# Kernel optimization log

Measured on AMD Instinct MI355X. Metric: run time of the kernel, lower is better.

Reference implementation:

```python
import jax, jax.numpy as jnp
import numpy as np

B, S, D, H = 4, 2048, 512, 8
DEPTH = D // H


def setup_inputs() -> dict:
    key = jax.random.key(0)
    ks = jax.random.split(key, 12)
    scale = 0.02
    inp = {
        "q": jax.random.normal(ks[0], (B, S, D), dtype=jnp.float32),
        "k": jax.random.normal(ks[1], (B, S, D), dtype=jnp.float32),
        "v": jax.random.normal(ks[2], (B, S, D), dtype=jnp.float32),
        "mask": jax.random.randint(ks[3], (B, S, S), 0, 2, dtype=jnp.int32),
        "wq": jax.random.normal(ks[4], (D, D), dtype=jnp.float32) * scale,
        "bq": jnp.zeros((D,), dtype=jnp.float32),
        "wk": jax.random.normal(ks[5], (D, D), dtype=jnp.float32) * scale,
        "bk": jnp.zeros((D,), dtype=jnp.float32),
        "wv": jax.random.normal(ks[6], (D, D), dtype=jnp.float32) * scale,
        "bv": jnp.zeros((D,), dtype=jnp.float32),
        "wo": jax.random.normal(ks[7], (D, D), dtype=jnp.float32) * scale,
        "bo": jnp.zeros((D,), dtype=jnp.float32),
    }
    return inp


def _split_heads(x):
    # [B, S, D] -> [B, H, S, depth]
    b, s, _ = x.shape
    return x.reshape(b, s, H, DEPTH).transpose(0, 2, 1, 3)


def reference(q, k, v, mask, wq, bq, wk, bk, wv, bv, wo, bo):
    qh = _split_heads(q @ wq + bq)
    kh = _split_heads(k @ wk + bk)
    vh = _split_heads(v @ wv + bv)
    # scaled dot-product attention with additive mask, materializing [B,H,S,S]
    scores = jnp.einsum("bhqd,bhkd->bhqk", qh, kh) / jnp.sqrt(
        jnp.asarray(DEPTH, jnp.float32)
    )
    scores = scores + mask[:, None, :, :].astype(jnp.float32) * (-1e9)
    w = jax.nn.softmax(scores, axis=-1)
    o = jnp.einsum("bhqk,bhkd->bhqd", w, vh)
    o = o.transpose(0, 2, 1, 3).reshape(q.shape[0], -1, D)  # [B, S, D]
    return o @ wo + bo
```

## Files before the change

kernel.cpp:

```cpp
#include <hip/hip_runtime.h>
#include <hip/hip_bf16.h>
#include <stdint.h>

#define B_ 4
#define S_ 2048
#define D_ 512
#define H_ 8

typedef __attribute__((ext_vector_type(8))) short short8;
typedef __attribute__((ext_vector_type(4))) float f32x4;
typedef __attribute__((ext_vector_type(4))) unsigned short u16x4;

#define MFMA16(a,b,c) __builtin_amdgcn_mfma_f32_16x16x32_bf16((a),(b),(c),0,0,0)

__device__ __forceinline__ unsigned short f2bf(float f){
    return __builtin_bit_cast(unsigned short, __float2bfloat16(f));
}

__device__ __forceinline__ float maskf(float p, uint32_t keep){
    return __builtin_bit_cast(float, __builtin_bit_cast(uint32_t, p) & keep);
}

__device__ __forceinline__ float max3f(float a, float b, float c){
    float d;
    asm("v_max3_f32 %0, %1, %2, %3" : "=v"(d) : "v"(a), "v"(b), "v"(c));
    return d;
}

__device__ __forceinline__ void gload_lds16(const void* g, void* l){
    __builtin_amdgcn_global_load_lds((const __attribute__((address_space(1))) uint32_t*)g,
                                     (__attribute__((address_space(3))) uint32_t*)l, 16, 0, 0);
}

__global__ __launch_bounds__(256) void maskpack_kernel(const int* __restrict__ mask,
                                                       uint32_t* __restrict__ out)
{
    int idx = blockIdx.x*256 + threadIdx.x;
    const int4* p = (const int4*)(mask + (size_t)idx*32);
    uint32_t bits = 0;
    #pragma unroll
    for (int c=0;c<8;c++){
        int4 v = p[c];
        if (v.x) bits |= 1u << (c*4+0);
        if (v.y) bits |= 1u << (c*4+1);
        if (v.z) bits |= 1u << (c*4+2);
        if (v.w) bits |= 1u << (c*4+3);
    }
    out[idx] = bits;
}

__global__ __launch_bounds__(256) void wtrans_kernel(const float* __restrict__ wq,
                                                     const float* __restrict__ wk,
                                                     const float* __restrict__ wv,
                                                     const float* __restrict__ wo,
                                                     unsigned short* __restrict__ wt)
{
    int f = (blockIdx.x*256 + threadIdx.x) * 8;
    int mat = f >> 18;
    int rem = f & 262143;
    const float* Wm = (mat==0)?wq:(mat==1)?wk:(mat==2)?wv:wo;
    int nn = rem >> 9, kk0 = rem & 511;
    short8 o;
    #pragma unroll
    for (int j=0;j<8;j++)
        o[j] = (short)f2bf(Wm[(size_t)(kk0+j)*512 + nn]);
    *(short8*)(wt + (size_t)mat*262144 + (size_t)nn*512 + kk0) = o;
}

__global__ __launch_bounds__(256) void proj_kernel(
    const float* __restrict__ q, const float* __restrict__ k, const float* __restrict__ v,
    const float* __restrict__ bq, const float* __restrict__ bk, const float* __restrict__ bv,
    const unsigned short* __restrict__ wt, unsigned short* __restrict__ outb)
{
    __shared__ uint8_t smem[16384];
    const int t = threadIdx.x, l = t&63, w = t>>6, g = l>>4, ln = l&15;
    const int z = blockIdx.z;
    const float* X = (z==0)? q : (z==1)? k : v;
    const float* bias = (z==0)? bq : (z==1)? bk : bv;
    const unsigned short* WTz = wt + (size_t)z*(D_*D_);
    unsigned short* out = outb + (size_t)z*((size_t)B_*H_*S_*64);
    const float scale = (z==0)? 0.18033688011112042f : 1.0f;
    const int m0 = blockIdx.x*128, n0 = blockIdx.y*128;
    uint8_t* As = smem; uint8_t* Bs = smem + 8192;
    const int RB = (w>>1)*64, CB = (w&1)*64;

    const f32x4 zz = {0.f,0.f,0.f,0.f};
    f32x4 acc[4][4];
    #pragma unroll
    for (int i=0;i<4;i++)
        #pragma unroll
        for (int j=0;j<4;j++) acc[i][j] = zz;

    for (int k0=0; k0<D_; k0+=32){
        __syncthreads();
        #pragma unroll
        for (int i=0;i<2;i++){
            int qc = w + i*4;
            int row = qc*16 + (l>>2);
            int colb = ((l&3)*16) ^ ((row&3)<<4);
            gload_lds16((const uint8_t*)WTz + (((size_t)(n0+row)*D_ + k0)<<1) + colb,
                        Bs + qc*1024);
        }
        #pragma unroll
        for (int i=0;i<2;i++){
            int c = t + i*256;
            int row = c>>2, cc = c&3;
            const float4* src = (const float4*)(X + (size_t)(m0+row)*D_ + k0 + cc*8);
            float4 u0 = src[0], u1 = src[1];
            uint32_t c0,c1,c2,c3;
            asm("v_cvt_pk_bf16_f32 %0, %1, %2" : "=v"(c0) : "v"(u0.x), "v"(u0.y));
            asm("v_cvt_pk_bf16_f32 %0, %1, %2" : "=v"(c1) : "v"(u0.z), "v"(u0.w));
            asm("v_cvt_pk_bf16_f32 %0, %1, %2" : "=v"(c2) : "v"(u1.x), "v"(u1.y));
            asm("v_cvt_pk_bf16_f32 %0, %1, %2" : "=v"(c3) : "v"(u1.z), "v"(u1.w));
            uint4 pk4; pk4.x=c0; pk4.y=c1; pk4.z=c2; pk4.w=c3;
            *(uint4*)(As + row*64 + ((cc*16) ^ ((row&3)<<4))) = pk4;
        }
        __syncthreads();
        short8 af[4], bfr[4];
        #pragma unroll
        for (int ai=0; ai<4; ai++){
            int row = RB + 16*ai + ln;
            af[ai] = *(const short8*)(As + row*64 + ((16*g) ^ ((row&3)<<4)));
        }
        #pragma unroll
        for (int bj=0; bj<4; bj++){
            int row = CB + 16*bj + ln;
            bfr[bj] = *(const short8*)(Bs + row*64 + ((16*g) ^ ((row&3)<<4)));
        }
        #pragma unroll
        for (int ai=0; ai<4; ai++)
            #pragma unroll
            for (int bj=0; bj<4; bj++)
                acc[ai][bj] = MFMA16(af[ai], bfr[bj], acc[ai][bj]);
    }

    if (z == 2){
        #pragma unroll
        for (int bj=0; bj<4; bj++){
            int gn = n0 + CB + 16*bj + ln;
            float bv2 = bias[gn];
            #pragma unroll
            for (int ai=0; ai<4; ai++){
                int gmb = m0 + RB + 16*ai + 4*g;
                int bidx = gmb >> 11, s = gmb & 2047;
                u16x4 pk;
                #pragma unroll
                for (int r=0;r<4;r++) pk[r] = f2bf(acc[ai][bj][r] + bv2);
                *(u16x4*)(out + ((size_t)bidx*D_ + gn)*S_ + s) = pk;
            }
        }
    } else {
        #pragma unroll
        for (int bj=0; bj<4; bj++){
            int gn = n0 + CB + 16*bj + ln;
            float bv2 = bias[gn];
            int h = gn >> 6, dep = gn & 63;
            #pragma unroll
            for (int ai=0; ai<4; ai++){
                #pragma unroll
                for (int r=0;r<4;r++){
                    int gm = m0 + RB + 16*ai + 4*g + r;
                    float val = (acc[ai][bj][r] + bv2) * scale;
                    size_t o = ((size_t)(gm>>11)*H_ + h)*((size_t)S_*64) + (size_t)(gm&2047)*64 + dep;
                    out[o] = f2bf(val);
                }
            }
        }
    }
}

__global__ __launch_bounds__(256) void attn_kernel(
    const unsigned short* __restrict__ qb, const unsigned short* __restrict__ kb,
    const unsigned short* __restrict__ vtb, const uint32_t* __restrict__ mb,
    unsigned short* __restrict__ ao)
{
    __shared__ uint8_t smem[40960];
    const int t = threadIdx.x, l = t&63, w = t>>6, g = l>>4, ln = l&15;
    const int bh = blockIdx.y;
    const int b = bh >> 3;
    const int q0 = blockIdx.x * 64;
    const unsigned short* Q  = qb + (size_t)bh*((size_t)S_*64);
    const unsigned short* K  = kb + (size_t)bh*((size_t)S_*64);
    const unsigned short* VT = vtb + ((size_t)b*D_ + (bh&7)*64)*S_;

    const int qrow = q0 + 16*w + ln;
    const short8 qf0 = *(const short8*)(Q + (size_t)qrow*64 + 8*g);
    const short8 qf1 = *(const short8*)(Q + (size_t)qrow*64 + 8*g + 32);

    const int Msw = (ln&7)<<4;
    const int sw0 = (16*g) ^ Msw;
    const int sw1 = (16*g + 64) ^ Msw;
    uint8_t* kB0 = smem + (ln*128 + sw0);
    uint8_t* kB1 = smem + (ln*128 + sw1);
    uint8_t* Pw = smem + 32768 + w*2048;
    uint8_t* prd0 = Pw + ln*128 + sw0;
    uint8_t* prd1 = Pw + ln*128 + sw1;

    int krow0 = w*8 + (l>>3), krow1 = (w+4)*8 + (l>>3);
    int colb0 = ((l&7)*16) ^ ((krow0&7)<<4);
    int colb1 = ((l&7)*16) ^ ((krow1&7)<<4);
    int kof0 = krow0*128 + colb0,     kof1 = krow1*128 + colb1;
    int vof0 = krow0*(S_*2) + colb0,  vof1 = krow1*(S_*2) + colb1;
    const int ldo0 = w*1024, ldo1 = (w+4)*1024;

    const uint2* mptr = (const uint2*)(mb + ((size_t)b*S_ + qrow)*64);

    const f32x4 zz = {0.f,0.f,0.f,0.f};
    f32x4 O[4], O5 = zz;
    #pragma unroll
    for (int i=0;i<4;i++) O[i] = zz;
    float c = 0.f;

    const short8 ones = {0x3F80,0x3F80,0x3F80,0x3F80,0x3F80,0x3F80,0x3F80,0x3F80};

    gload_lds16((const uint8_t*)K  + kof0, smem + ldo0);
    gload_lds16((const uint8_t*)K  + kof1, smem + ldo1);
    gload_lds16((const uint8_t*)VT + vof0, smem + 16384 + ldo0);
    gload_lds16((const uint8_t*)VT + vof1, smem + 16384 + ldo1);
    kof0 += 8192; kof1 += 8192; vof0 += 128; vof1 += 128;
    int curb = 0;
    uint2 mmc = mptr[0];

    for (int it=0; it<S_/64; ++it){
        __syncthreads();
        if (it < S_/64 - 1){
            int nx = curb ^ 8192;
            gload_lds16((const uint8_t*)K  + kof0, smem + nx + ldo0);
            gload_lds16((const uint8_t*)K  + kof1, smem + nx + ldo1);
            gload_lds16((const uint8_t*)VT + vof0, smem + 16384 + nx + ldo0);
            gload_lds16((const uint8_t*)VT + vof1, smem + 16384 + nx + ldo1);
            kof0 += 8192; kof1 += 8192; vof0 += 128; vof1 += 128;
        }
        uint2 mmn = mptr[(it+1)&31];
        const uint8_t* b0 = kB0 + curb;
        const uint8_t* b1 = kB1 + curb;

        f32x4 st[4];
        __builtin_amdgcn_s_setprio(1);
        #pragma unroll
        for (int t4=0;t4<4;t4++){
            short8 kf0 = *(const short8*)(b0 + 2048*t4);
            short8 kf1 = *(const short8*)(b1 + 2048*t4);
            st[t4] = MFMA16(kf0, qf0, zz);
            st[t4] = MFMA16(kf1, qf1, st[t4]);
        }
        __builtin_amdgcn_s_setprio(0);

        float m0a = max3f(st[0][0], st[0][1], st[0][2]);
        float m1a = max3f(st[0][3], st[1][0], st[1][1]);
        float m2a = max3f(st[1][2], st[1][3], st[2][0]);
        float m3a = max3f(st[2][1], st[2][2], st[2][3]);
        float m4a = max3f(st[3][0], st[3][1], st[3][2]);
        float lmax = fmaxf(max3f(m0a, m1a, m2a), max3f(m3a, m4a, st[3][3]));
        if (__builtin_expect(__any(lmax > c + 8.0f), 0)){
            float rm = lmax;
            rm = fmaxf(rm, __shfl_xor(rm, 16));
            rm = fmaxf(rm, __shfl_xor(rm, 32));
            float cnew = fmaxf(c, rm);
            float al = __builtin_amdgcn_exp2f(c - cnew);
            c = cnew;
            #pragma unroll
            for (int r=0;r<4;r++){
                float aO = __shfl(al, 4*g + r);
                #pragma unroll
                for (int db=0; db<4; db++) O[db][r] *= aO;
                O5[r] *= aO;
            }
        }

        uint32_t mi0 = (~mmc.x) >> (4*g);
        uint32_t mi1 = (~mmc.y) >> (4*g);
        #pragma unroll
        for (int t4=0;t4<4;t4++){
            uint32_t mi = (t4 >= 2) ? mi1 : mi0;
            const int sh = (t4&1)*16;
            float p0 = maskf(__builtin_amdgcn_exp2f(st[t4][0] - c),
                             (uint32_t)(((int32_t)(mi << (31-(sh+0)))) >> 31));
            float p1 = maskf(__builtin_amdgcn_exp2f(st[t4][1] - c),
                             (uint32_t)(((int32_t)(mi << (31-(sh+1)))) >> 31));
            float p2 = maskf(__builtin_amdgcn_exp2f(st[t4][2] - c),
                             (uint32_t)(((int32_t)(mi << (31-(sh+2)))) >> 31));
            float p3 = maskf(__builtin_amdgcn_exp2f(st[t4][3] - c),
                             (uint32_t)(((int32_t)(mi << (31-(sh+3)))) >> 31));
            uint32_t lo, hi;
            asm("v_cvt_pk_bf16_f32 %0, %1, %2" : "=v"(lo) : "v"(p0), "v"(p1));
            asm("v_cvt_pk_bf16_f32 %0, %1, %2" : "=v"(hi) : "v"(p2), "v"(p3));
            uint2 pk; pk.x = lo; pk.y = hi;
            *(uint2*)(Pw + ln*128 + ((32*t4 + 8*g) ^ Msw)) = pk;
        }
        mmc = mmn;

        asm volatile("s_waitcnt lgkmcnt(0)" ::: "memory");

        short8 pa0 = *(const short8*)prd0;
        short8 pa1 = *(const short8*)prd1;
        __builtin_amdgcn_s_setprio(1);
        #pragma unroll
        for (int db=0; db<4; db++){
            short8 vf0 = *(const short8*)(b0 + 16384 + 2048*db);
            short8 vf1 = *(const short8*)(b1 + 16384 + 2048*db);
            O[db] = MFMA16(pa0, vf0, O[db]);
            O[db] = MFMA16(pa1, vf1, O[db]);
        }
        O5 = MFMA16(pa0, ones, O5);
        O5 = MFMA16(pa1, ones, O5);
        __builtin_amdgcn_s_setprio(0);
        curb ^= 8192;
    }

    #pragma unroll
    for (int r=0;r<4;r++){
        float inv = 1.0f / O5[r];
        int gm = b*S_ + q0 + 16*w + 4*g + r;
        #pragma unroll
        for (int db=0; db<4; db++){
            int col = (bh&7)*64 + 16*db + ln;
            ao[(size_t)gm*D_ + col] = f2bf(O[db][r]*inv);
        }
    }
}

__global__ __launch_bounds__(256) void outproj_kernel(
    const unsigned short* __restrict__ ao, const unsigned short* __restrict__ wt,
    const float* __restrict__ bo, float* __restrict__ out)
{
    __shared__ uint8_t smem[16384];
    const int t = threadIdx.x, l = t&63, w = t>>6, g = l>>4, ln = l&15;
    const unsigned short* WTz = wt + (size_t)3*(D_*D_);
    const int m0 = blockIdx.x*128, n0 = blockIdx.y*128;
    uint8_t* As = smem; uint8_t* Bs = smem + 8192;
    const int RB = (w>>1)*64, CB = (w&1)*64;

    const f32x4 zz = {0.f,0.f,0.f,0.f};
    f32x4 acc[4][4];
    #pragma unroll
    for (int i=0;i<4;i++)
        #pragma unroll
        for (int j=0;j<4;j++) acc[i][j] = zz;

    for (int k0=0; k0<D_; k0+=32){
        __syncthreads();
        #pragma unroll
        for (int i=0;i<2;i++){
            int qc = w + i*4;
            int row = qc*16 + (l>>2);
            int colb = ((l&3)*16) ^ ((row&3)<<4);
            gload_lds16((const uint8_t*)WTz + (((size_t)(n0+row)*D_ + k0)<<1) + colb,
                        Bs + qc*1024);
            gload_lds16((const uint8_t*)ao + (((size_t)(m0+row)*D_ + k0)<<1) + colb,
                        As + qc*1024);
        }
        __syncthreads();
        short8 af[4], bfr[4];
        #pragma unroll
        for (int ai=0; ai<4; ai++){
            int row = RB + 16*ai + ln;
            af[ai] = *(const short8*)(As + row*64 + ((16*g) ^ ((row&3)<<4)));
        }
        #pragma unroll
        for (int bj=0; bj<4; bj++){
            int row = CB + 16*bj + ln;
            bfr[bj] = *(const short8*)(Bs + row*64 + ((16*g) ^ ((row&3)<<4)));
        }
        #pragma unroll
        for (int ai=0; ai<4; ai++)
            #pragma unroll
            for (int bj=0; bj<4; bj++)
                acc[ai][bj] = MFMA16(af[ai], bfr[bj], acc[ai][bj]);
    }

    #pragma unroll
    for (int bj=0; bj<4; bj++){
        int gn = n0 + CB + 16*bj + ln;
        float bv2 = bo[gn];
        #pragma unroll
        for (int ai=0; ai<4; ai++){
            #pragma unroll
            for (int r=0;r<4;r++){
                int gm = m0 + RB + 16*ai + 4*g + r;
                out[(size_t)gm*D_ + gn] = acc[ai][bj][r] + bv2;
            }
        }
    }
}

extern "C" void kernel_launch(void* const* d_in, const int* in_sizes, int n_in,
                              void* d_out, int out_size, void* d_ws, size_t ws_size,
                              hipStream_t stream)
{
    const float* q  = (const float*)d_in[0];
    const float* k  = (const float*)d_in[1];
    const float* v  = (const float*)d_in[2];
    const int* mask = (const int*)d_in[3];
    const float* wq = (const float*)d_in[4];
    const float* bq = (const float*)d_in[5];
    const float* wk = (const float*)d_in[6];
    const float* bk = (const float*)d_in[7];
    const float* wv = (const float*)d_in[8];
    const float* bv = (const float*)d_in[9];
    const float* wo = (const float*)d_in[10];
    const float* bo = (const float*)d_in[11];

    uint8_t* ws = (uint8_t*)d_ws;
    unsigned short* qkvb = (unsigned short*)ws;
    unsigned short* ao   = (unsigned short*)(ws + 25165824);
    unsigned short* wt   = (unsigned short*)(ws + 33554432);
    uint32_t*       mb   = (uint32_t*)      (ws + 35651584);
    float* out = (float*)d_out;

    maskpack_kernel<<<dim3(2048), dim3(256), 0, stream>>>(mask, mb);
    wtrans_kernel<<<dim3(512), dim3(256), 0, stream>>>(wq, wk, wv, wo, wt);
    proj_kernel<<<dim3(64,4,3), dim3(256), 0, stream>>>(q, k, v, bq, bk, bv, wt, qkvb);
    attn_kernel<<<dim3(32,32), dim3(256), 0, stream>>>(qkvb, qkvb + 4194304, qkvb + 8388608, mb, ao);
    outproj_kernel<<<dim3(64,4), dim3(256), 0, stream>>>(ao, wt, bo, out);
}
```

Before: 140.6 us.

## Feed P straight from registers into 16x16x16 MFMA and rework projections

The attention kernel now keeps the softmax probabilities in registers and consumes them with the 16x16x16 bf16 MFMA, which accepts the accumulator layout of the QK product directly. This removes the LDS round trip and lgkmcnt wait for P and shrinks shared memory, so launch bounds can request 4 blocks per SIMD. A wave-uniform fast path skips subtracting the running max while it is still zero, and mask bits are extracted with sbfe. The V projection swaps MFMA operand order and changes how it writes its output, and the weight transpose switches to one element per thread. The smaller MFMA shape issues more instructions per unit of work, and the new V and weight-transpose stores are scalar and may coalesce poorly.

```diff
diff --git a/kernel.cpp b/kernel.cpp
--- a/kernel.cpp
+++ b/kernel.cpp
@@ -8,10 +8,24 @@
 #define H_ 8
 
 typedef __attribute__((ext_vector_type(8))) short short8;
+typedef __attribute__((ext_vector_type(4))) short short4v;
 typedef __attribute__((ext_vector_type(4))) float f32x4;
 typedef __attribute__((ext_vector_type(4))) unsigned short u16x4;
 
 #define MFMA16(a,b,c) __builtin_amdgcn_mfma_f32_16x16x32_bf16((a),(b),(c),0,0,0)
+
+#if __has_builtin(__builtin_amdgcn_mfma_f32_16x16x16bf16_1k)
+#define HAVE16K 1
+#define MFMA16K(a,b,c) __builtin_amdgcn_mfma_f32_16x16x16bf16_1k((a),(b),(c),0,0,0)
+#else
+#define HAVE16K 0
+#endif
+
+#if __has_builtin(__builtin_amdgcn_sbfe)
+#define SBFE1(v, off) ((uint32_t)__builtin_amdgcn_sbfe((int)(v), (off), 1))
+#else
+#define SBFE1(v, off) ((uint32_t)(((int32_t)((v) << (31-(off)))) >> 31))
+#endif
 
 __device__ __forceinline__ unsigned short f2bf(float f){
     return __builtin_bit_cast(unsigned short, __float2bfloat16(f));
@@ -55,16 +69,12 @@
                                                      const float* __restrict__ wo,
                                                      unsigned short* __restrict__ wt)
 {
-    int f = (blockIdx.x*256 + threadIdx.x) * 8;
+    int f = blockIdx.x*256 + threadIdx.x;
     int mat = f >> 18;
     int rem = f & 262143;
     const float* Wm = (mat==0)?wq:(mat==1)?wk:(mat==2)?wv:wo;
-    int nn = rem >> 9, kk0 = rem & 511;
-    short8 o;
-    #pragma unroll
-    for (int j=0;j<8;j++)
-        o[j] = (short)f2bf(Wm[(size_t)(kk0+j)*512 + nn]);
-    *(short8*)(wt + (size_t)mat*262144 + (size_t)nn*512 + kk0) = o;
+    int kk = rem >> 9, nn = rem & 511;
+    wt[(size_t)mat*262144 + (size_t)nn*512 + kk] = f2bf(Wm[rem]);
 }
 
 __global__ __launch_bounds__(256) void proj_kernel(
@@ -127,26 +137,33 @@
             int row = CB + 16*bj + ln;
             bfr[bj] = *(const short8*)(Bs + row*64 + ((16*g) ^ ((row&3)<<4)));
         }
-        #pragma unroll
-        for (int ai=0; ai<4; ai++)
-            #pragma unroll
-            for (int bj=0; bj<4; bj++)
-                acc[ai][bj] = MFMA16(af[ai], bfr[bj], acc[ai][bj]);
+        if (z == 2){
+            #pragma unroll
+            for (int ai=0; ai<4; ai++)
+                #pragma unroll
+                for (int bj=0; bj<4; bj++)
+                    acc[ai][bj] = MFMA16(bfr[bj], af[ai], acc[ai][bj]);
+        } else {
+            #pragma unroll
+            for (int ai=0; ai<4; ai++)
+                #pragma unroll
+                for (int bj=0; bj<4; bj++)
+                    acc[ai][bj] = MFMA16(af[ai], bfr[bj], acc[ai][bj]);
+        }
     }
 
     if (z == 2){
         #pragma unroll
         for (int bj=0; bj<4; bj++){
-            int gn = n0 + CB + 16*bj + ln;
-            float bv2 = bias[gn];
             #pragma unroll
             for (int ai=0; ai<4; ai++){
-                int gmb = m0 + RB + 16*ai + 4*g;
-                int bidx = gmb >> 11, s = gmb & 2047;
-                u16x4 pk;
+                int s = m0 + RB + 16*ai + ln;
                 #pragma unroll
-                for (int r=0;r<4;r++) pk[r] = f2bf(acc[ai][bj][r] + bv2);
-                *(u16x4*)(out + ((size_t)bidx*D_ + gn)*S_ + s) = pk;
+                for (int r=0;r<4;r++){
+                    int gn = n0 + CB + 16*bj + 4*g + r;
+                    float val = acc[ai][bj][r] + bias[gn];
+                    out[((size_t)(s>>11)*D_ + gn)*S_ + (s&2047)] = f2bf(val);
+                }
             }
         }
     } else {
@@ -169,12 +186,16 @@
     }
 }
 
-__global__ __launch_bounds__(256) void attn_kernel(
+__global__ __launch_bounds__(256, 4) void attn_kernel(
     const unsigned short* __restrict__ qb, const unsigned short* __restrict__ kb,
     const unsigned short* __restrict__ vtb, const uint32_t* __restrict__ mb,
     unsigned short* __restrict__ ao)
 {
+#if HAVE16K
+    __shared__ uint8_t smem[32768];
+#else
     __shared__ uint8_t smem[40960];
+#endif
     const int t = threadIdx.x, l = t&63, w = t>>6, g = l>>4, ln = l&15;
     const int bh = blockIdx.y;
     const int b = bh >> 3;
@@ -190,11 +211,19 @@
     const int Msw = (ln&7)<<4;
     const int sw0 = (16*g) ^ Msw;
     const int sw1 = (16*g + 64) ^ Msw;
-    uint8_t* kB0 = smem + (ln*128 + sw0);
-    uint8_t* kB1 = smem + (ln*128 + sw1);
+    uint8_t* kB0 = smem + ln*128 + sw0;
+    uint8_t* kB1 = smem + ln*128 + sw1;
+#if HAVE16K
+    uint8_t* vB  = smem + 16384 + ln*128;
+    const int vo0 = (8*g     ) ^ Msw;
+    const int vo1 = (8*g + 32) ^ Msw;
+    const int vo2 = (8*g + 64) ^ Msw;
+    const int vo3 = (8*g + 96) ^ Msw;
+#else
     uint8_t* Pw = smem + 32768 + w*2048;
     uint8_t* prd0 = Pw + ln*128 + sw0;
     uint8_t* prd1 = Pw + ln*128 + sw1;
+#endif
 
     int krow0 = w*8 + (l>>3), krow1 = (w+4)*8 + (l>>3);
     int colb0 = ((l&7)*16) ^ ((krow0&7)<<4);
@@ -211,7 +240,10 @@
     for (int i=0;i<4;i++) O[i] = zz;
     float c = 0.f;
 
-    const short8 ones = {0x3F80,0x3F80,0x3F80,0x3F80,0x3F80,0x3F80,0x3F80,0x3F80};
+    const short4v onesv = {0x3F80,0x3F80,0x3F80,0x3F80};
+#if !HAVE16K
+    const short8 ones8 = {0x3F80,0x3F80,0x3F80,0x3F80,0x3F80,0x3F80,0x3F80,0x3F80};
+#endif
 
     gload_lds16((const uint8_t*)K  + kof0, smem + ldo0);
     gload_lds16((const uint8_t*)K  + kof1, smem + ldo1);
@@ -270,41 +302,67 @@
 
         uint32_t mi0 = (~mmc.x) >> (4*g);
         uint32_t mi1 = (~mmc.y) >> (4*g);
+        short4v pa[4];
+        auto genp = [&](float cc){
+            #pragma unroll
+            for (int t4=0;t4<4;t4++){
+                uint32_t mi = (t4 >= 2) ? mi1 : mi0;
+                const int base = (t4&1)*16;
+                float p0 = maskf(__builtin_amdgcn_exp2f(st[t4][0] - cc), SBFE1(mi, base+0));
+                float p1 = maskf(__builtin_amdgcn_exp2f(st[t4][1] - cc), SBFE1(mi, base+1));
+                float p2 = maskf(__builtin_amdgcn_exp2f(st[t4][2] - cc), SBFE1(mi, base+2));
+                float p3 = maskf(__builtin_amdgcn_exp2f(st[t4][3] - cc), SBFE1(mi, base+3));
+                uint32_t lo, hi;
+                asm("v_cvt_pk_bf16_f32 %0, %1, %2" : "=v"(lo) : "v"(p0), "v"(p1));
+                asm("v_cvt_pk_bf16_f32 %0, %1, %2" : "=v"(hi) : "v"(p2), "v"(p3));
+                uint2 u; u.x = lo; u.y = hi;
+                pa[t4] = __builtin_bit_cast(short4v, u);
+            }
+        };
+        if (__builtin_expect(__all(c == 0.0f), 1)) genp(0.0f); else genp(c);
+        mmc = mmn;
+
+#if HAVE16K
+        __builtin_amdgcn_s_setprio(1);
+        const uint8_t* vb = vB + curb;
+        #pragma unroll
+        for (int db=0; db<4; db++){
+            short4v vf0 = *(const short4v*)(vb + 2048*db + vo0);
+            short4v vf1 = *(const short4v*)(vb + 2048*db + vo1);
+            short4v vf2 = *(const short4v*)(vb + 2048*db + vo2);
+            short4v vf3 = *(const short4v*)(vb + 2048*db + vo3);
+            O[db] = MFMA16K(pa[0], vf0, O[db]);
+            O[db] = MFMA16K(pa[1], vf1, O[db]);
+            O[db] = MFMA16K(pa[2], vf2, O[db]);
+            O[db] = MFMA16K(pa[3], vf3, O[db]);
+        }
+        O5 = MFMA16K(pa[0], onesv, O5);
+        O5 = MFMA16K(pa[1], onesv, O5);
+        O5 = MFMA16K(pa[2], onesv, O5);
+        O5 = MFMA16K(pa[3], onesv, O5);
+        __builtin_amdgcn_s_setprio(0);
+#else
         #pragma unroll
         for (int t4=0;t4<4;t4++){
-            uint32_t mi = (t4 >= 2) ? mi1 : mi0;
-            const int sh = (t4&1)*16;
-            float p0 = maskf(__builtin_amdgcn_exp2f(st[t4][0] - c),
-                             (uint32_t)(((int32_t)(mi << (31-(sh+0)))) >> 31));
-            float p1 = maskf(__builtin_amdgcn_exp2f(st[t4][1] - c),
-                             (uint32_t)(((int32_t)(mi << (31-(sh+1)))) >> 31));
-            float p2 = maskf(__builtin_amdgcn_exp2f(st[t4][2] - c),
-                             (uint32_t)(((int32_t)(mi << (31-(sh+2)))) >> 31));
-            float p3 = maskf(__builtin_amdgcn_exp2f(st[t4][3] - c),
-                             (uint32_t)(((int32_t)(mi << (31-(sh+3)))) >> 31));
-            uint32_t lo, hi;
-            asm("v_cvt_pk_bf16_f32 %0, %1, %2" : "=v"(lo) : "v"(p0), "v"(p1));
-            asm("v_cvt_pk_bf16_f32 %0, %1, %2" : "=v"(hi) : "v"(p2), "v"(p3));
-            uint2 pk; pk.x = lo; pk.y = hi;
-            *(uint2*)(Pw + ln*128 + ((32*t4 + 8*g) ^ Msw)) = pk;
-        }
-        mmc = mmn;
-
+            uint2 u = __builtin_bit_cast(uint2, pa[t4]);
+            *(uint2*)(Pw + ln*128 + ((32*t4 + 8*g) ^ Msw)) = u;
+        }
         asm volatile("s_waitcnt lgkmcnt(0)" ::: "memory");
-
         short8 pa0 = *(const short8*)prd0;
         short8 pa1 = *(const short8*)prd1;
         __builtin_amdgcn_s_setprio(1);
         #pragma unroll
         for (int db=0; db<4; db++){
-            short8 vf0 = *(const short8*)(b0 + 16384 + 2048*db);
-            short8 vf1 = *(const short8*)(b1 + 16384 + 2048*db);
+            int dr = 16*db + ln;
+            short8 vf0 = *(const short8*)(smem + 16384 + curb + dr*128 + ((16*g     ) ^ ((dr&7)<<4)));
+            short8 vf1 = *(const short8*)(smem + 16384 + curb + dr*128 + ((16*g + 64) ^ ((dr&7)<<4)));
             O[db] = MFMA16(pa0, vf0, O[db]);
             O[db] = MFMA16(pa1, vf1, O[db]);
         }
-        O5 = MFMA16(pa0, ones, O5);
-        O5 = MFMA16(pa1, ones, O5);
+        O5 = MFMA16(pa0, ones8, O5);
+        O5 = MFMA16(pa1, ones8, O5);
         __builtin_amdgcn_s_setprio(0);
+#endif
         curb ^= 8192;
     }
 
@@ -409,7 +467,7 @@
     float* out = (float*)d_out;
 
     maskpack_kernel<<<dim3(2048), dim3(256), 0, stream>>>(mask, mb);
-    wtrans_kernel<<<dim3(512), dim3(256), 0, stream>>>(wq, wk, wv, wo, wt);
+    wtrans_kernel<<<dim3(4096), dim3(256), 0, stream>>>(wq, wk, wv, wo, wt);
     proj_kernel<<<dim3(64,4,3), dim3(256), 0, stream>>>(q, k, v, bq, bk, bv, wt, qkvb);
     attn_kernel<<<dim3(32,32), dim3(256), 0, stream>>>(qkvb, qkvb + 4194304, qkvb + 8388608, mb, ao);
     outproj_kernel<<<dim3(64,4), dim3(256), 0, stream>>>(ao, wt, bo, out);
```

After: 135.0 us. 4.0% less time.
